# Optimization experiments

Measured on AMD Instinct MI355X. Metric: run time of the kernel, lower is better.

## Reference

```python
import jax, jax.numpy as jnp
import numpy as np

N_NODES = 50000
N_EDGES = 640000
IN_FEATS = 512
HID = 128
OUT_FEATS = 128
N_GRAPHS = 256


def setup_inputs() -> dict:
    key = jax.random.key(0)
    ks = jax.random.split(key, 7)
    x = jax.random.normal(ks[0], (N_NODES, IN_FEATS), dtype=jnp.float32)
    edge_index = jax.random.randint(ks[1], (2, N_EDGES), 0, N_NODES, dtype=jnp.int32)
    batch = jnp.sort(jax.random.randint(ks[2], (N_NODES,), 0, N_GRAPHS, dtype=jnp.int32))
    W1 = jax.random.normal(ks[3], (IN_FEATS, HID), dtype=jnp.float32) * (1.0 / np.sqrt(IN_FEATS))
    b1 = jnp.zeros((HID,), jnp.float32)
    W2 = jax.random.normal(ks[4], (HID, OUT_FEATS), dtype=jnp.float32) * (1.0 / np.sqrt(HID))
    b2 = jnp.zeros((OUT_FEATS,), jnp.float32)
    return {"x": x, "W1": W1, "b1": b1, "W2": W2, "b2": b2,
            "edge_index": edge_index, "batch": batch}


def reference(x, W1, b1, W2, b2, edge_index, batch):
    N = x.shape[0]
    loop = jnp.arange(N, dtype=edge_index.dtype)
    # PyG GCNConv default: add self-loops, symmetric deg^-1/2 normalization
    row = jnp.concatenate([edge_index[0], loop])  # source
    col = jnp.concatenate([edge_index[1], loop])  # target
    deg = jax.ops.segment_sum(jnp.ones_like(col, x.dtype), col, num_segments=N)
    dinv = jnp.where(deg > 0, jax.lax.rsqrt(deg), 0.0)
    norm = dinv[row] * dinv[col]  # [E+N]

    def gcn_conv(h, W, b):
        h = h @ W  # linear transform first (PyG order)
        msg = h[row] * norm[:, None]  # gather + scale
        agg = jax.ops.segment_sum(msg, col, num_segments=N)  # scatter-add
        return agg + b

    h = jax.nn.relu(gcn_conv(x, W1, b1))  # dropout is identity in eval mode
    h = gcn_conv(h, W2, b2)
    hs = jax.ops.segment_sum(h, batch, num_segments=N_GRAPHS)  # global_add_pool
    return hs, h
```

## Files before the change

### kernel.cpp

```cpp
#include <hip/hip_runtime.h>
#include <hip/hip_bf16.h>

#define N_NODES  50000
#define N_EDGES  640000
#define IN_FEATS 512
#define HID      128
#define OUT_FEATS 128
#define N_GRAPHS 256

#define SCAN_CHUNK 1024
#define SCAN_BLOCKS ((N_NODES + SCAN_CHUNK - 1) / SCAN_CHUNK)

typedef __attribute__((ext_vector_type(8))) short short8;
typedef __attribute__((ext_vector_type(4))) float f32x4;

__device__ __forceinline__ float bf2f(unsigned u16) {
    return __uint_as_float(u16 << 16);
}
__device__ __forceinline__ unsigned short f2bf(float f) {
    __hip_bfloat16 h = __float2bfloat16(f);
    return *(unsigned short*)&h;
}

__device__ __forceinline__ short8 cvt8(float4 x, float4 y) {
    short8 r;
    r[0] = (short)f2bf(x.x); r[1] = (short)f2bf(x.y);
    r[2] = (short)f2bf(x.z); r[3] = (short)f2bf(x.w);
    r[4] = (short)f2bf(y.x); r[5] = (short)f2bf(y.y);
    r[6] = (short)f2bf(y.z); r[7] = (short)f2bf(y.w);
    return r;
}

__device__ __forceinline__ void gl_lds16(const void* g, void* l) {
    __builtin_amdgcn_global_load_lds(
        (const __attribute__((address_space(1))) void*)g,
        (__attribute__((address_space(3))) void*)l, 16, 0, 0);
}

#define PREP_BLOCKS 644

__global__ __launch_bounds__(256) void k_prep(const float* __restrict__ W1,
                                              const float* __restrict__ W2,
                                              unsigned short* __restrict__ wt1,
                                              unsigned short* __restrict__ wt2,
                                              int* __restrict__ cnt,
                                              float* __restrict__ hs) {
    int b = blockIdx.x;
    int t = threadIdx.x;
    if (b < 196) {
        int i = b * 256 + t;
        if (i < N_NODES) cnt[i] = 0;
    } else if (b < 452) {
        int idx = (b - 196) * 256 + t;
        int n = idx & 127, k = idx >> 7;
        wt1[(size_t)n * IN_FEATS + k] = f2bf(W1[(size_t)k * 128 + n]);
    } else if (b < 516) {
        int idx = (b - 452) * 256 + t;
        int n = idx & 127, k = idx >> 7;
        wt2[(size_t)n * HID + k] = f2bf(W2[(size_t)k * 128 + n]);
    } else {
        int idx = (b - 516) * 256 + t;
        hs[idx] = 0.f;
    }
}


template <int K>
__global__ __launch_bounds__(256, 2) void k_g1c(const float* __restrict__ A,
                                                const unsigned short* __restrict__ Bt,
                                                unsigned short* __restrict__ Cb, int M,
                                                const int* __restrict__ col,
                                                int* __restrict__ cnt, int nblk_gemm) {
    __shared__ float          As[2][64][64];
    __shared__ unsigned short Bs[2][128][64];
    int tid = threadIdx.x;

    if (blockIdx.x >= nblk_gemm) {
        int e4 = ((blockIdx.x - nblk_gemm) * 256 + tid) * 4;
        if (e4 < N_EDGES) {
            int4 c = *(const int4*)(col + e4);
            atomicAdd(&cnt[c.x], 1);
            atomicAdd(&cnt[c.y], 1);
            atomicAdd(&cnt[c.z], 1);
            atomicAdd(&cnt[c.w], 1);
        }
        return;
    }

    int wave = tid >> 6;
    int lane = tid & 63;
    int quad = lane >> 4;
    int l15 = lane & 15;
    int wm = wave >> 1;
    int wn = wave & 1;
    int m0 = blockIdx.x * 64;

#define STAGE(buf, k0) {                                                        \
    _Pragma("unroll")                                                           \
    for (int is = 0; is < 4; ++is) {                                            \
        int a_ = wave * 4 + is;                             \
        int c = a_ * 64 + lane;                              \
        int r = c >> 4, pcol = c & 15;                                          \
        int lcol = pcol ^ (r & 7);                                              \
        int gr = m0 + r; if (gr >= M) gr = M - 1;                               \
        const float* g = A + (size_t)gr * K + (k0) + lcol * 4;                  \
        void* l = (char*)&As[buf][0][0] + a_ * 1024;                            \
        gl_lds16(g, l);                                                         \
    }                                                                           \
    _Pragma("unroll")                                                           \
    for (int is = 0; is < 4; ++is) {                                            \
        int a_ = wave * 4 + is;                                                 \
        int c = a_ * 64 + lane;                                                 \
        int r = c >> 3, pcol = c & 7;                                           \
        int lcol = pcol ^ (r & 7);                                              \
        const unsigned short* g = Bt + (size_t)r * K + (k0) + lcol * 8;         \
        void* l = (char*)&Bs[buf][0][0] + a_ * 1024;                            \
        gl_lds16(g, l);                                                         \
    }                                                                           \
}

    f32x4 acc[2][4];
#pragma unroll
    for (int i = 0; i < 2; ++i)
#pragma unroll
        for (int j = 0; j < 4; ++j) acc[i][j] = (f32x4){0.f, 0.f, 0.f, 0.f};

    const int NT = K / 64;
    STAGE(0, 0);
    STAGE(1, 64);

#pragma unroll 1
    for (int t = 0; t < NT; ++t) {
        int buf = t & 1;
        if (t == NT - 1) { asm volatile("s_waitcnt vmcnt(0)" ::: "memory"); }
        else             { asm volatile("s_waitcnt vmcnt(8)" ::: "memory"); }
        __builtin_amdgcn_s_barrier();

        const char* abase = (const char*)&As[buf][0][0];
        const char* bbase = (const char*)&Bs[buf][0][0];
        float4 ax[2][2], ay[2][2];
#pragma unroll
        for (int kh = 0; kh < 2; ++kh)
#pragma unroll
            for (int i = 0; i < 2; ++i) {
                int r = wm * 32 + i * 16 + l15;
                int lc = kh * 8 + quad * 2;
                int p0 = lc ^ (r & 7);
                ax[kh][i] = *(const float4*)(abase + r * 256 + p0 * 16);
                ay[kh][i] = *(const float4*)(abase + r * 256 + (p0 ^ 1) * 16);
            }
        short8 bfr[2][4];
#pragma unroll
        for (int kh = 0; kh < 2; ++kh)
#pragma unroll
            for (int j = 0; j < 4; ++j) {
                int r = wn * 64 + j * 16 + l15;
                int lc = kh * 4 + quad;
                int p = lc ^ (r & 7);
                bfr[kh][j] = *(const short8*)(bbase + r * 128 + p * 16);
            }

        asm volatile("s_waitcnt lgkmcnt(0)" ::: "memory");
        __builtin_amdgcn_sched_barrier(0);
        __builtin_amdgcn_s_barrier();

        if (t < NT - 2) STAGE(buf, (t + 2) * 64);
        __builtin_amdgcn_sched_barrier(0);

#pragma unroll
        for (int kh = 0; kh < 2; ++kh) {
            short8 a0 = cvt8(ax[kh][0], ay[kh][0]);
            short8 a1 = cvt8(ax[kh][1], ay[kh][1]);
#pragma unroll
            for (int j = 0; j < 4; ++j) {
                acc[0][j] = __builtin_amdgcn_mfma_f32_16x16x32_bf16(a0, bfr[kh][j], acc[0][j], 0, 0, 0);
                acc[1][j] = __builtin_amdgcn_mfma_f32_16x16x32_bf16(a1, bfr[kh][j], acc[1][j], 0, 0, 0);
            }
        }
    }
#undef STAGE

#pragma unroll
    for (int i = 0; i < 2; ++i) {
        int rb = m0 + wm * 32 + i * 16 + quad * 4;
#pragma unroll
        for (int j = 0; j < 4; ++j) {
            int colb = wn * 64 + j * 16 + l15;
#pragma unroll
            for (int r2 = 0; r2 < 4; ++r2) {
                int gm = rb + r2;
                if (gm < M) Cb[(size_t)gm * 128 + colb] = f2bf(acc[i][j][r2]);
            }
        }
    }
}


__global__ __launch_bounds__(256) void k_scan_a(const int* __restrict__ cnt,
                                                int* __restrict__ offs,
                                                int* __restrict__ bsum) {
    __shared__ int sums[256];
    int t = threadIdx.x;
    int base = blockIdx.x * SCAN_CHUNK + t * 4;
    int c0 = 0, c1 = 0, c2 = 0, c3 = 0;
    if (base + 3 < N_NODES) {
        int4 v = *(const int4*)(cnt + base);
        c0 = v.x; c1 = v.y; c2 = v.z; c3 = v.w;
    } else {
        if (base + 0 < N_NODES) c0 = cnt[base + 0];
        if (base + 1 < N_NODES) c1 = cnt[base + 1];
        if (base + 2 < N_NODES) c2 = cnt[base + 2];
    }
    int ts = c0 + c1 + c2 + c3;
    sums[t] = ts;
    __syncthreads();
#pragma unroll
    for (int off = 1; off < 256; off <<= 1) {
        int add = (t >= off) ? sums[t - off] : 0;
        __syncthreads();
        sums[t] += add;
        __syncthreads();
    }
    int ex = sums[t] - ts;
    if (base + 3 < N_NODES) {
        int4 o;
        o.x = ex; o.y = ex + c0; o.z = ex + c0 + c1; o.w = ex + c0 + c1 + c2;
        *(int4*)(offs + base) = o;
    } else {
        if (base + 0 < N_NODES) offs[base + 0] = ex;
        if (base + 1 < N_NODES) offs[base + 1] = ex + c0;
        if (base + 2 < N_NODES) offs[base + 2] = ex + c0 + c1;
    }
    if (t == 255) bsum[blockIdx.x] = sums[255];
}

__global__ __launch_bounds__(256) void k_scan_c(const int* __restrict__ cnt,
                                                const int* __restrict__ bsum,
                                                int* __restrict__ offs,
                                                int* __restrict__ cursor,
                                                float* __restrict__ dinv) {
    __shared__ int sb[64];
    int t = threadIdx.x;
    int b = blockIdx.x;
    if (t < 64) sb[t] = (t < SCAN_BLOCKS) ? bsum[t] : 0;
    __syncthreads();
#pragma unroll
    for (int off = 1; off < 64; off <<= 1) {
        int add = 0;
        if (t < 64 && t >= off) add = sb[t - off];
        __syncthreads();
        if (t < 64) sb[t] += add;
        __syncthreads();
    }
    int add = (b == 0) ? 0 : sb[b - 1];
    int base = b * SCAN_CHUNK + t * 4;
    if (base + 3 < N_NODES) {
        int4 o = *(const int4*)(offs + base);
        o.x += add; o.y += add; o.z += add; o.w += add;
        *(int4*)(offs + base) = o;
        *(int4*)(cursor + base) = o;
        int4 c = *(const int4*)(cnt + base);
        float4 d;
        d.x = rsqrtf((float)c.x + 1.0f);
        d.y = rsqrtf((float)c.y + 1.0f);
        d.z = rsqrtf((float)c.z + 1.0f);
        d.w = rsqrtf((float)c.w + 1.0f);
        *(float4*)(dinv + base) = d;
    } else {
#pragma unroll
        for (int j = 0; j < 4; ++j) {
            int i = base + j;
            if (i < N_NODES) {
                int o = offs[i] + add;
                offs[i] = o; cursor[i] = o;
                dinv[i] = rsqrtf((float)cnt[i] + 1.0f);
            }
        }
    }
    if (b == 0 && t == 0) offs[N_NODES] = N_EDGES;
}

__global__ void k_fill(const int* __restrict__ row, const int* __restrict__ col,
                       int* __restrict__ cursor, int* __restrict__ srcIdx) {
    int e4 = (blockIdx.x * blockDim.x + threadIdx.x) * 4;
    if (e4 >= N_EDGES) return;
    int4 r = *(const int4*)(row + e4);
    int4 c = *(const int4*)(col + e4);
    srcIdx[atomicAdd(&cursor[c.x], 1)] = r.x;
    srcIdx[atomicAdd(&cursor[c.y], 1)] = r.y;
    srcIdx[atomicAdd(&cursor[c.z], 1)] = r.z;
    srcIdx[atomicAdd(&cursor[c.w], 1)] = r.w;
}


template <int RELU>
__global__ __launch_bounds__(256) void k_agg(const unsigned* __restrict__ t,
                                             const int* __restrict__ offs,
                                             const int* __restrict__ srcIdx,
                                             const float* __restrict__ dinv,
                                             const float* __restrict__ bias,
                                             unsigned* __restrict__ out_) {
    int wave = threadIdx.x >> 6;
    int lane = threadIdx.x & 63;
    int h = lane >> 5;
    int l = lane & 31;
    int i = blockIdx.x * 4 + wave;
    float di = dinv[i];
    const unsigned* my = t + (size_t)i * 64 + 2 * l;

    float s0 = 0.f, s1 = 0.f, s2 = 0.f, s3 = 0.f;
    {
        uint2 sv = *(const uint2*)my;
        if (h == 0) {
            s0 = bf2f(sv.x & 0xffffu) * di;
            s1 = bf2f(sv.x >> 16) * di;
            s2 = bf2f(sv.y & 0xffffu) * di;
            s3 = bf2f(sv.y >> 16) * di;
        }
    }
    int lo = offs[i], hi = offs[i + 1];
    for (int e = lo; e < hi; e += 16) {
        int idx[8];
        float d[8];
        uint2 v[8];
#pragma unroll
        for (int j = 0; j < 8; ++j) {
            int ee = e + 2 * j + h;
            idx[j] = (ee < hi) ? srcIdx[ee] : i;
        }
#pragma unroll
        for (int j = 0; j < 8; ++j)
            v[j] = *(const uint2*)(t + (size_t)idx[j] * 64 + 2 * l);
#pragma unroll
        for (int j = 0; j < 8; ++j) {
            int ee = e + 2 * j + h;
            d[j] = (ee < hi) ? dinv[idx[j]] : 0.f;
        }
#pragma unroll
        for (int j = 0; j < 8; ++j) {
            s0 = fmaf(bf2f(v[j].x & 0xffffu), d[j], s0);
            s1 = fmaf(bf2f(v[j].x >> 16),     d[j], s1);
            s2 = fmaf(bf2f(v[j].y & 0xffffu), d[j], s2);
            s3 = fmaf(bf2f(v[j].y >> 16),     d[j], s3);
        }
    }
    s0 += __shfl_xor(s0, 32);
    s1 += __shfl_xor(s1, 32);
    s2 += __shfl_xor(s2, 32);
    s3 += __shfl_xor(s3, 32);

    float r0 = s0 * di, r1 = s1 * di, r2 = s2 * di, r3 = s3 * di;
    if (bias) {
        float4 bb = *(const float4*)(bias + 4 * l);
        r0 += bb.x; r1 += bb.y; r2 += bb.z; r3 += bb.w;
    }
    if (RELU) {
        r0 = fmaxf(r0, 0.f); r1 = fmaxf(r1, 0.f);
        r2 = fmaxf(r2, 0.f); r3 = fmaxf(r3, 0.f);
    }
    if (h == 0) {
        uint2 o;
        o.x = (unsigned)f2bf(r0) | ((unsigned)f2bf(r1) << 16);
        o.y = (unsigned)f2bf(r2) | ((unsigned)f2bf(r3) << 16);
        *(uint2*)(out_ + (size_t)i * 64 + 2 * l) = o;
    }
}


__global__ __launch_bounds__(256) void k_gemm2_pool(const unsigned short* __restrict__ G,
                                                    const unsigned short* __restrict__ Bt,
                                                    const float* __restrict__ bias,
                                                    const int* __restrict__ batch,
                                                    float* __restrict__ out,
                                                    float* __restrict__ hs, int M) {
    const int K = HID;
    __shared__ unsigned short As[4][64][8];
    __shared__ unsigned short Bs[4][128][8];
    int tid = threadIdx.x;
    int wave = tid >> 6;
    int lane = tid & 63;
    int quad = lane >> 4;
    int l15 = lane & 15;
    int m0 = blockIdx.x * 64;

    f32x4 acc[8];
#pragma unroll
    for (int nt = 0; nt < 8; ++nt) acc[nt] = (f32x4){0.f, 0.f, 0.f, 0.f};

    int gm_a = m0 + lane; if (gm_a >= M) gm_a = M - 1;
    const unsigned short* ap_base = G + (size_t)gm_a * K + wave * 8;

    for (int k0 = 0; k0 < K; k0 += 32) {
        *(short8*)&As[wave][lane][0] = *(const short8*)(ap_base + k0);
#pragma unroll
        for (int i = 0; i < 2; ++i) {
            int slot = tid + i * 256;
            int bkq = slot >> 7;
            int n = slot & 127;
            *(short8*)&Bs[bkq][n][0] = *(const short8*)(Bt + (size_t)n * K + k0 + bkq * 8);
        }
        __syncthreads();
        short8 a = *(short8*)&As[quad][wave * 16 + l15][0];
#pragma unroll
        for (int nt = 0; nt < 8; ++nt) {
            short8 b = *(short8*)&Bs[quad][nt * 16 + l15][0];
            acc[nt] = __builtin_amdgcn_mfma_f32_16x16x32_bf16(a, b, acc[nt], 0, 0, 0);
        }
        __syncthreads();
    }
    int rb = m0 + wave * 16 + quad * 4;
    int g_[4];
#pragma unroll
    for (int r2 = 0; r2 < 4; ++r2)
        g_[r2] = (rb + r2 < M) ? batch[rb + r2] : -1;
#pragma unroll
    for (int nt = 0; nt < 8; ++nt) {
        int colb = nt * 16 + l15;
        float bcol = bias[colb];
        float v[4];
#pragma unroll
        for (int r2 = 0; r2 < 4; ++r2) {
            v[r2] = acc[nt][r2] + bcol;
            if (rb + r2 < M) out[(size_t)(rb + r2) * 128 + colb] = v[r2];
        }
        float run = v[0];
        int gcur = g_[0];
#pragma unroll
        for (int r2 = 1; r2 < 4; ++r2) {
            if (g_[r2] == gcur) run += v[r2];
            else {
                if (gcur >= 0) atomicAdd(&hs[(size_t)gcur * 128 + colb], run);
                gcur = g_[r2]; run = v[r2];
            }
        }
        if (gcur >= 0) atomicAdd(&hs[(size_t)gcur * 128 + colb], run);
    }
}


extern "C" void kernel_launch(void* const* d_in, const int* in_sizes, int n_in,
                              void* d_out, int out_size, void* d_ws, size_t ws_size,
                              hipStream_t stream) {
    const float* x  = (const float*)d_in[0];
    const float* W1 = (const float*)d_in[1];
    const float* b1 = (const float*)d_in[2];
    const float* W2 = (const float*)d_in[3];
    const float* b2 = (const float*)d_in[4];
    const int*   ei = (const int*)d_in[5];
    const int*   batch = (const int*)d_in[6];
    const int* row = ei;
    const int* col = ei + N_EDGES;

    float* out_hs = (float*)d_out;
    float* out_h  = (float*)d_out + N_GRAPHS * OUT_FEATS;

    char* ws = (char*)d_ws;
    unsigned short* tb   = (unsigned short*)ws;
    unsigned short* h1b  = (unsigned short*)(ws + 12800000);
    unsigned short* gb   = (unsigned short*)(ws + 25600000);
    float* dinv = (float*)(ws + 38400000);
    int*   cnt    = (int*)(ws + 38600000);
    int*   offs   = (int*)(ws + 38800000);
    int*   cursor = (int*)(ws + 39000016);
    int*   srcIdx = (int*)(ws + 39200016);
    int*   bsum   = (int*)(ws + 41761056);
    unsigned short* wt1 = (unsigned short*)(ws + 41761472);
    unsigned short* wt2 = (unsigned short*)(ws + 41892544);

    const int TB = 256;
    const int GB1 = (N_NODES + 63) / 64;
    const int CB  = (N_EDGES / 4 + TB - 1) / TB;

    k_prep<<<PREP_BLOCKS, 256, 0, stream>>>(W1, W2, wt1, wt2, cnt, out_hs);
    k_g1c<IN_FEATS><<<GB1 + CB, 256, 0, stream>>>(x, wt1, tb, N_NODES, col, cnt, GB1);
    k_scan_a<<<SCAN_BLOCKS, 256, 0, stream>>>(cnt, offs, bsum);
    k_scan_c<<<SCAN_BLOCKS, 256, 0, stream>>>(cnt, bsum, offs, cursor, dinv);
    k_fill<<<(N_EDGES / 4 + TB - 1) / TB, TB, 0, stream>>>(row, col, cursor, srcIdx);

    k_agg<1><<<N_NODES / 4, 256, 0, stream>>>((const unsigned*)tb, offs, srcIdx, dinv, b1, (unsigned*)h1b);
    k_agg<0><<<N_NODES / 4, 256, 0, stream>>>((const unsigned*)h1b, offs, srcIdx, dinv, nullptr, (unsigned*)gb);
    k_gemm2_pool<<<(N_NODES + 63) / 64, 256, 0, stream>>>(gb, wt2, b2, batch, out_h, out_hs, N_NODES);
}
```

Before: 321.3 us.

## Widen aggregation loads to 16B per lane and stage full-K gemm2 tiles in swizzled LDS

The aggregation kernel now has each lane load 8 bf16 features (uint4) so a 16-lane group covers a 128-feature row, with four edges in flight per wave instead of two. The partial sums are combined with two xor-shuffles. The second GEMM now loads the whole K=128 tile of A (through a global-to-LDS helper) and of B into XOR-swizzled shared memory once. This removes the per-k-step sync loop and LDS bank conflicts. The trade-off is larger LDS use per block, limited by launch_bounds(256,3), plus higher register pressure in the aggregation kernel.

```diff
diff --git a/kernel.cpp b/kernel.cpp
--- a/kernel.cpp
+++ b/kernel.cpp
@@ -302,80 +302,88 @@
                                              unsigned* __restrict__ out_) {
     int wave = threadIdx.x >> 6;
     int lane = threadIdx.x & 63;
-    int h = lane >> 5;
-    int l = lane & 31;
+    int g = lane >> 4;
+    int l16 = lane & 15;
     int i = blockIdx.x * 4 + wave;
     float di = dinv[i];
-    const unsigned* my = t + (size_t)i * 64 + 2 * l;
-
-    float s0 = 0.f, s1 = 0.f, s2 = 0.f, s3 = 0.f;
+
+    float s[8];
     {
-        uint2 sv = *(const uint2*)my;
-        if (h == 0) {
-            s0 = bf2f(sv.x & 0xffffu) * di;
-            s1 = bf2f(sv.x >> 16) * di;
-            s2 = bf2f(sv.y & 0xffffu) * di;
-            s3 = bf2f(sv.y >> 16) * di;
-        }
+        uint4 sv = *((const uint4*)(t + (size_t)i * 64) + l16);
+        float w = (g == 0) ? di : 0.f;
+        s[0] = bf2f(sv.x & 0xffffu) * w; s[1] = bf2f(sv.x >> 16) * w;
+        s[2] = bf2f(sv.y & 0xffffu) * w; s[3] = bf2f(sv.y >> 16) * w;
+        s[4] = bf2f(sv.z & 0xffffu) * w; s[5] = bf2f(sv.z >> 16) * w;
+        s[6] = bf2f(sv.w & 0xffffu) * w; s[7] = bf2f(sv.w >> 16) * w;
     }
     int lo = offs[i], hi = offs[i + 1];
     for (int e = lo; e < hi; e += 16) {
-        int idx[8];
-        float d[8];
-        uint2 v[8];
-#pragma unroll
-        for (int j = 0; j < 8; ++j) {
-            int ee = e + 2 * j + h;
+        int idx[4];
+        float d[4];
+        uint4 v[4];
+#pragma unroll
+        for (int j = 0; j < 4; ++j) {
+            int ee = e + 4 * j + g;
             idx[j] = (ee < hi) ? srcIdx[ee] : i;
         }
 #pragma unroll
-        for (int j = 0; j < 8; ++j)
-            v[j] = *(const uint2*)(t + (size_t)idx[j] * 64 + 2 * l);
-#pragma unroll
-        for (int j = 0; j < 8; ++j) {
-            int ee = e + 2 * j + h;
+        for (int j = 0; j < 4; ++j)
+            v[j] = *((const uint4*)(t + (size_t)idx[j] * 64) + l16);
+#pragma unroll
+        for (int j = 0; j < 4; ++j) {
+            int ee = e + 4 * j + g;
             d[j] = (ee < hi) ? dinv[idx[j]] : 0.f;
         }
 #pragma unroll
-        for (int j = 0; j < 8; ++j) {
-            s0 = fmaf(bf2f(v[j].x & 0xffffu), d[j], s0);
-            s1 = fmaf(bf2f(v[j].x >> 16),     d[j], s1);
-            s2 = fmaf(bf2f(v[j].y & 0xffffu), d[j], s2);
-            s3 = fmaf(bf2f(v[j].y >> 16),     d[j], s3);
-        }
-    }
-    s0 += __shfl_xor(s0, 32);
-    s1 += __shfl_xor(s1, 32);
-    s2 += __shfl_xor(s2, 32);
-    s3 += __shfl_xor(s3, 32);
-
-    float r0 = s0 * di, r1 = s1 * di, r2 = s2 * di, r3 = s3 * di;
+        for (int j = 0; j < 4; ++j) {
+            s[0] = fmaf(bf2f(v[j].x & 0xffffu), d[j], s[0]);
+            s[1] = fmaf(bf2f(v[j].x >> 16),     d[j], s[1]);
+            s[2] = fmaf(bf2f(v[j].y & 0xffffu), d[j], s[2]);
+            s[3] = fmaf(bf2f(v[j].y >> 16),     d[j], s[3]);
+            s[4] = fmaf(bf2f(v[j].z & 0xffffu), d[j], s[4]);
+            s[5] = fmaf(bf2f(v[j].z >> 16),     d[j], s[5]);
+            s[6] = fmaf(bf2f(v[j].w & 0xffffu), d[j], s[6]);
+            s[7] = fmaf(bf2f(v[j].w >> 16),     d[j], s[7]);
+        }
+    }
+#pragma unroll
+    for (int k = 0; k < 8; ++k) {
+        s[k] += __shfl_xor(s[k], 16);
+        s[k] += __shfl_xor(s[k], 32);
+    }
+
+    float r[8];
+#pragma unroll
+    for (int k = 0; k < 8; ++k) r[k] = s[k] * di;
     if (bias) {
-        float4 bb = *(const float4*)(bias + 4 * l);
-        r0 += bb.x; r1 += bb.y; r2 += bb.z; r3 += bb.w;
+        float4 b0 = *(const float4*)(bias + 8 * l16);
+        float4 b1 = *(const float4*)(bias + 8 * l16 + 4);
+        r[0] += b0.x; r[1] += b0.y; r[2] += b0.z; r[3] += b0.w;
+        r[4] += b1.x; r[5] += b1.y; r[6] += b1.z; r[7] += b1.w;
     }
     if (RELU) {
-        r0 = fmaxf(r0, 0.f); r1 = fmaxf(r1, 0.f);
-        r2 = fmaxf(r2, 0.f); r3 = fmaxf(r3, 0.f);
-    }
-    if (h == 0) {
-        uint2 o;
-        o.x = (unsigned)f2bf(r0) | ((unsigned)f2bf(r1) << 16);
-        o.y = (unsigned)f2bf(r2) | ((unsigned)f2bf(r3) << 16);
-        *(uint2*)(out_ + (size_t)i * 64 + 2 * l) = o;
-    }
-}
-
-
-__global__ __launch_bounds__(256) void k_gemm2_pool(const unsigned short* __restrict__ G,
-                                                    const unsigned short* __restrict__ Bt,
-                                                    const float* __restrict__ bias,
-                                                    const int* __restrict__ batch,
-                                                    float* __restrict__ out,
-                                                    float* __restrict__ hs, int M) {
-    const int K = HID;
-    __shared__ unsigned short As[4][64][8];
-    __shared__ unsigned short Bs[4][128][8];
+#pragma unroll
+        for (int k = 0; k < 8; ++k) r[k] = fmaxf(r[k], 0.f);
+    }
+    if (lane < 16) {
+        uint4 o;
+        o.x = (unsigned)f2bf(r[0]) | ((unsigned)f2bf(r[1]) << 16);
+        o.y = (unsigned)f2bf(r[2]) | ((unsigned)f2bf(r[3]) << 16);
+        o.z = (unsigned)f2bf(r[4]) | ((unsigned)f2bf(r[5]) << 16);
+        o.w = (unsigned)f2bf(r[6]) | ((unsigned)f2bf(r[7]) << 16);
+        *((uint4*)(out_ + (size_t)i * 64) + l16) = o;
+    }
+}
+
+
+__global__ __launch_bounds__(256, 3) void k_gemm2_pool(const unsigned short* __restrict__ G,
+                                                       const unsigned short* __restrict__ Bt,
+                                                       const float* __restrict__ bias,
+                                                       const int* __restrict__ batch,
+                                                       float* __restrict__ out,
+                                                       float* __restrict__ hs, int M) {
+    __shared__ unsigned short As[64][128];
+    __shared__ unsigned short Bs[128][128];
     int tid = threadIdx.x;
     int wave = tid >> 6;
     int lane = tid & 63;
@@ -383,31 +391,45 @@
     int l15 = lane & 15;
     int m0 = blockIdx.x * 64;
 
+#pragma unroll
+    for (int is = 0; is < 4; ++is) {
+        int a_ = wave * 4 + is;
+        int c = a_ * 64 + lane;
+        int r = c >> 4, pcol = c & 15;
+        int lcol = pcol ^ (r & 7);
+        int gr = m0 + r; if (gr >= M) gr = M - 1;
+        const unsigned short* gp = G + (size_t)gr * 128 + lcol * 8;
+        void* l = (char*)&As[0][0] + a_ * 1024;
+        gl_lds16(gp, l);
+    }
+#pragma unroll
+    for (int it = 0; it < 8; ++it) {
+        int idx = it * 256 + tid;
+        int n = idx >> 4, lc = idx & 15;
+        int p = lc ^ (n & 7);
+        *(uint4*)((char*)&Bs[0][0] + n * 256 + p * 16) =
+            *(const uint4*)(Bt + (size_t)n * 128 + lc * 8);
+    }
+    asm volatile("s_waitcnt vmcnt(0)" ::: "memory");
+    __syncthreads();
+
     f32x4 acc[8];
 #pragma unroll
     for (int nt = 0; nt < 8; ++nt) acc[nt] = (f32x4){0.f, 0.f, 0.f, 0.f};
 
-    int gm_a = m0 + lane; if (gm_a >= M) gm_a = M - 1;
-    const unsigned short* ap_base = G + (size_t)gm_a * K + wave * 8;
-
-    for (int k0 = 0; k0 < K; k0 += 32) {
-        *(short8*)&As[wave][lane][0] = *(const short8*)(ap_base + k0);
-#pragma unroll
-        for (int i = 0; i < 2; ++i) {
-            int slot = tid + i * 256;
-            int bkq = slot >> 7;
-            int n = slot & 127;
-            *(short8*)&Bs[bkq][n][0] = *(const short8*)(Bt + (size_t)n * K + k0 + bkq * 8);
-        }
-        __syncthreads();
-        short8 a = *(short8*)&As[quad][wave * 16 + l15][0];
+    int ra = wave * 16 + l15;
+#pragma unroll
+    for (int s = 0; s < 4; ++s) {
+        int kc = s * 4 + quad;
+        short8 a = *(const short8*)((char*)&As[0][0] + ra * 256 + (kc ^ (ra & 7)) * 16);
 #pragma unroll
         for (int nt = 0; nt < 8; ++nt) {
-            short8 b = *(short8*)&Bs[quad][nt * 16 + l15][0];
+            int rn = nt * 16 + l15;
+            short8 b = *(const short8*)((char*)&Bs[0][0] + rn * 256 + (kc ^ (rn & 7)) * 16);
             acc[nt] = __builtin_amdgcn_mfma_f32_16x16x32_bf16(a, b, acc[nt], 0, 0, 0);
         }
-        __syncthreads();
-    }
+    }
+
     int rb = m0 + wave * 16 + quad * 4;
     int g_[4];
 #pragma unroll
```

After: 309.2 us. 1.04x faster.
